# Performance work log

Measured on AMD Instinct MI355X. Metric: run time of the kernel, lower is better.

## Reference

```python
import jax, jax.numpy as jnp
import numpy as np

N, E, H, HEADS, NC, BLK = 100000, 1600000, 128, 4, 8192, 128

def _layernorm(x, g, b, eps=1e-5):
    m = jnp.mean(x, axis=-1, keepdims=True)
    v = jnp.var(x, axis=-1, keepdims=True)
    return (x - m) * jax.lax.rsqrt(v + eps) * g + b

def setup_inputs() -> dict:
    key = jax.random.key(0)
    ks = jax.random.split(key, 24)
    s = 0.05
    p = lambda k, shp: jax.random.normal(k, shp, jnp.float32) * s
    return {
        'x': jax.random.normal(ks[0], (N, H), jnp.float32),
        'ea': jax.random.normal(ks[1], (E, H), jnp.float32),
        # GINEConv edge linear (edge_dim -> hidden)
        'We': p(ks[2], (H, H)), 'be_': p(ks[3], (H,)),
        # GINEConv mlp: Linear(H,H) -> ReLU -> Linear(H,H)
        'W1': p(ks[4], (H, H)), 'b1': p(ks[5], (H,)),
        'W2': p(ks[6], (H, H)), 'b2': p(ks[7], (H,)),
        'ln1_g': jnp.ones((H,), jnp.float32), 'ln1_b': jnp.zeros((H,), jnp.float32),
        # MultiheadAttention packed qkv + out proj
        'in_w': p(ks[8], (3 * H, H)), 'in_b': p(ks[9], (3 * H,)),
        'out_w': p(ks[10], (H, H)), 'out_b': p(ks[11], (H,)),
        'ln2_g': jnp.ones((H,), jnp.float32), 'ln2_b': jnp.zeros((H,), jnp.float32),
        # FFN: Linear(H,2H) -> ReLU -> Linear(2H,H)
        'f1_w': p(ks[12], (2 * H, H)), 'f1_b': p(ks[13], (2 * H,)),
        'f2_w': p(ks[14], (H, 2 * H)), 'f2_b': p(ks[15], (H,)),
        'ei': jax.random.randint(ks[16], (2, E), 0, N, jnp.int64),
        'chem_idx': jnp.arange(NC, dtype=jnp.int64),
        'B': BLK,
    }

def reference(x, ea, We, be_, W1, b1, W2, b2, ln1_g, ln1_b, in_w, in_b,
              out_w, out_b, ln2_g, ln2_b, f1_w, f1_b, f2_w, f2_b,
              ei, chem_idx, B):
    n = x.shape[0]
    # ---- GINEConv: out_i = mlp((1+eps)*x_i + sum_j relu(x_j + lin(e_ji))), eps=0 ----
    src, dst = ei[0], ei[1]
    msg = jax.nn.relu(x[src] + ea @ We.T + be_)          # [E, H]
    agg = jax.ops.segment_sum(msg, dst, num_segments=n)  # [N, H]
    h = agg + x
    h = jax.nn.relu(h @ W1.T + b1) @ W2.T + b2
    x = _layernorm(x + h, ln1_g, ln1_b)
    # ---- chunked self-attention over chem nodes (chunks of size B) ----
    xc = x[chem_idx].reshape(-1, B, x.shape[-1])         # [nc, B, H]
    nc, _, hid = xc.shape
    dh = hid // HEADS
    qkv = xc @ in_w.T + in_b                             # [nc, B, 3H]
    q, k, v = jnp.split(qkv, 3, axis=-1)
    sp = lambda t: t.reshape(nc, B, HEADS, dh)
    att = jax.nn.softmax(jnp.einsum('bqhd,bkhd->bhqk', sp(q), sp(k)) * (1.0 / np.sqrt(dh)).astype(np.float32), axis=-1)
    o = jnp.einsum('bhqk,bkhd->bqhd', att, sp(v)).reshape(nc, B, hid)
    xc = xc + (o @ out_w.T + out_b)                      # residual inside BlockMHA
    xc = xc.reshape(-1, hid)
    # ---- FFN on chem subset ----
    h2 = _layernorm(xc, ln2_g, ln2_b)
    xc = xc + (jax.nn.relu(h2 @ f1_w.T + f1_b) @ f2_w.T + f2_b)
    return x.at[chem_idx].set(xc)
```

## Files before the change

kernel.cpp:

```cpp
#include <hip/hip_runtime.h>
#include <hip/hip_bf16.h>
#include <math.h>

typedef __attribute__((ext_vector_type(8))) __bf16 bf16x8;
typedef __attribute__((ext_vector_type(4))) float f32x4;
typedef __attribute__((ext_vector_type(4))) unsigned short u16x4;

#define HD  128
#define LDP 136

__device__ __forceinline__ unsigned short f2bf(float f) {
  __bf16 h = (__bf16)f;
  union { __bf16 h; unsigned short u; } v; v.h = h; return v.u;
}
__device__ __forceinline__ float bf2f(unsigned short h) {
  union { unsigned u; float f; } v; v.u = ((unsigned)h) << 16; return v.f;
}

__device__ __forceinline__ int idx_at(const void* p, long long i, int is64) {
  if (is64) return (int)((const long long*)p)[i];
  return ((const int*)p)[i];
}

__device__ __forceinline__ void mfma_tile_128(const unsigned short* a_s,
                                              const unsigned short* w_s,
                                              int w, int l15, int lg,
                                              f32x4 acc[2][8]) {
#pragma unroll
  for (int kk = 0; kk < 4; ++kk) {
    bf16x8 a[2], b[8];
#pragma unroll
    for (int mt = 0; mt < 2; ++mt)
      a[mt] = *(const bf16x8*)&a_s[(w * 32 + mt * 16 + l15) * LDP + kk * 32 + lg * 8];
#pragma unroll
    for (int nt = 0; nt < 8; ++nt)
      b[nt] = *(const bf16x8*)&w_s[(nt * 16 + l15) * LDP + kk * 32 + lg * 8];
#pragma unroll
    for (int mt = 0; mt < 2; ++mt)
#pragma unroll
      for (int nt = 0; nt < 8; ++nt)
        acc[mt][nt] = __builtin_amdgcn_mfma_f32_16x16x32_bf16(a[mt], b[nt], acc[mt][nt], 0, 0, 0);
  }
}

__device__ __forceinline__ void mfma_tile_gb(const unsigned short* a_s,
                                             const unsigned short* Wb,
                                             int w, int l15, int lg,
                                             f32x4 acc[2][8]) {
#pragma unroll
  for (int kk = 0; kk < 4; ++kk) {
    bf16x8 a[2], b[8];
#pragma unroll
    for (int mt = 0; mt < 2; ++mt)
      a[mt] = *(const bf16x8*)&a_s[(w * 32 + mt * 16 + l15) * LDP + kk * 32 + lg * 8];
#pragma unroll
    for (int nt = 0; nt < 8; ++nt)
      b[nt] = *(const bf16x8*)&Wb[(nt * 16 + l15) * 128 + kk * 32 + lg * 8];
#pragma unroll
    for (int mt = 0; mt < 2; ++mt)
#pragma unroll
      for (int nt = 0; nt < 8; ++nt)
        acc[mt][nt] = __builtin_amdgcn_mfma_f32_16x16x32_bf16(a[mt], b[nt], acc[mt][nt], 0, 0, 0);
  }
}

__device__ __forceinline__ void stage_f32s(unsigned short* dst, const float* src,
                                           long long src_ld, int tid, int T) {
  for (int i = tid; i < 128 * 32; i += T) {
    int r = i >> 5, c = (i & 31) << 2;
    float4 f = *(const float4*)&src[(long long)r * src_ld + c];
    u16x4 h = { f2bf(f.x), f2bf(f.y), f2bf(f.z), f2bf(f.w) };
    *(u16x4*)&dst[r * LDP + c] = h;
  }
}

__global__ void detect_idx_kernel(const void* __restrict__ ei, int E, int N,
                                  int* __restrict__ flag) {
  if (threadIdx.x == 0 && blockIdx.x == 0) {
    const long long* p = (const long long*)ei;
    int is64 = 1;
    long long step = E / 64; if (step < 1) step = 1;
    for (int i = 0; i < 64; ++i) {
      long long v = p[i * step];
      if (v < 0 || v >= N) { is64 = 0; break; }
    }
    *flag = is64;
  }
}

__global__ __launch_bounds__(256) void conv_we_kernel(const float* __restrict__ We,
                                                      unsigned short* __restrict__ we_bf) {
  int i = blockIdx.x * 256 + threadIdx.x;
  if (i < 128 * 128) {
    int r = i >> 7, c = i & 127;
    we_bf[r * 136 + c] = f2bf(We[i]);
  }
}
__global__ __launch_bounds__(256) void conv_w_kernel(const float* __restrict__ W,
                                                     unsigned short* __restrict__ out,
                                                     int n) {
  int i = blockIdx.x * 256 + threadIdx.x;
  if (i < n) out[i] = f2bf(W[i]);
}

__global__ __launch_bounds__(256) void hist_kernel(const void* __restrict__ ei,
                                                   const int* __restrict__ flag,
                                                   int* __restrict__ deg, int E) {
  const int is64 = *flag;
  for (long long e = blockIdx.x * 256LL + threadIdx.x; e < E;
       e += (long long)gridDim.x * 256)
    atomicAdd(&deg[idx_at(ei, (long long)E + e, is64)], 1);
}

#define SCH 1024
__global__ __launch_bounds__(256) void scan_a(const int* __restrict__ deg,
                                              int* __restrict__ bsum, int N) {
  const int b = blockIdx.x, t = threadIdx.x;
  int p = 0;
#pragma unroll
  for (int k = 0; k < 4; ++k) {
    int idx = b * SCH + t * 4 + k;
    if (idx < N) p += deg[idx];
  }
  __shared__ int warr[4];
  for (int o = 32; o > 0; o >>= 1) p += __shfl_xor(p, o);
  if ((t & 63) == 0) warr[t >> 6] = p;
  __syncthreads();
  if (t == 0) bsum[b] = warr[0] + warr[1] + warr[2] + warr[3];
}
__global__ void scan_b(int* __restrict__ bsum, int* __restrict__ off, int NB, int N) {
  if (threadIdx.x == 0 && blockIdx.x == 0) {
    int run = 0;
    for (int b = 0; b < NB; ++b) { int t = bsum[b]; bsum[b] = run; run += t; }
    off[N] = run;
  }
}
__global__ __launch_bounds__(256) void scan_c(const int* __restrict__ deg,
                                              const int* __restrict__ bsum,
                                              int* __restrict__ off,
                                              int* __restrict__ cursor, int N) {
  const int b = blockIdx.x, t = threadIdx.x;
  int d[4], s = 0;
#pragma unroll
  for (int k = 0; k < 4; ++k) {
    int idx = b * SCH + t * 4 + k;
    d[k] = (idx < N) ? deg[idx] : 0;
    s += d[k];
  }
  __shared__ int arr[256];
  arr[t] = s;
  __syncthreads();
  for (int stp = 1; stp < 256; stp <<= 1) {
    int v = (t >= stp) ? arr[t - stp] : 0;
    __syncthreads();
    arr[t] += v;
    __syncthreads();
  }
  int base = bsum[b] + arr[t] - s;
  int acc = 0;
#pragma unroll
  for (int k = 0; k < 4; ++k) {
    int idx = b * SCH + t * 4 + k;
    if (idx < N) { off[idx] = base + acc; cursor[idx] = base + acc; }
    acc += d[k];
  }
}

__global__ __launch_bounds__(256, 4) void edge_kernel8(
    const float* __restrict__ x, const float* __restrict__ ea,
    const unsigned short* __restrict__ we_bf, const float* __restrict__ be,
    const void* __restrict__ ei, const int* __restrict__ flag,
    int* __restrict__ cursor, unsigned short* __restrict__ msg, int E) {
  __shared__ unsigned short we_s[128 * LDP];
  __shared__ int s_src[128];
  __shared__ int s_pos[128];
  const int tid = threadIdx.x;
  const long long e0 = (long long)blockIdx.x * 128;
  const int is64 = *flag;

  if (tid < 128) {
    long long e = e0 + tid;
    int s = 0, p = 0;
    if (e < E) {
      s = idx_at(ei, e, is64);
      int d = idx_at(ei, (long long)E + e, is64);
      p = atomicAdd(&cursor[d], 1);
    }
    s_src[tid] = s; s_pos[tid] = p;
  }

  const int lane = tid & 63, w = tid >> 6;
  const int l15 = lane & 15, lg = lane >> 4;

  float4 af[2][4][2];
#pragma unroll
  for (int mt = 0; mt < 2; ++mt) {
    long long row = e0 + w * 32 + mt * 16 + l15;
    const float* src = &ea[(row < E ? row : e0) * HD + lg * 8];
#pragma unroll
    for (int kk = 0; kk < 4; ++kk) {
      af[mt][kk][0] = *(const float4*)&src[kk * 32];
      af[mt][kk][1] = *(const float4*)&src[kk * 32 + 4];
    }
  }

  for (int i = tid; i < 2048; i += 256) {
    int r = i >> 4, c = (i & 15) << 3;
    *(float4*)&we_s[r * LDP + c] = *(const float4*)&we_bf[r * 136 + c];
  }

  bf16x8 a[2][4];
#pragma unroll
  for (int mt = 0; mt < 2; ++mt)
#pragma unroll
    for (int kk = 0; kk < 4; ++kk) {
      float4 f0 = af[mt][kk][0], f1 = af[mt][kk][1];
      bf16x8 t;
      t[0] = (__bf16)f0.x; t[1] = (__bf16)f0.y; t[2] = (__bf16)f0.z; t[3] = (__bf16)f0.w;
      t[4] = (__bf16)f1.x; t[5] = (__bf16)f1.y; t[6] = (__bf16)f1.z; t[7] = (__bf16)f1.w;
      a[mt][kk] = t;
    }
  __syncthreads();

  f32x4 acc[2][8];
#pragma unroll
  for (int mt = 0; mt < 2; ++mt)
#pragma unroll
    for (int nt = 0; nt < 8; ++nt) acc[mt][nt] = (f32x4){0.f, 0.f, 0.f, 0.f};

#pragma unroll
  for (int kk = 0; kk < 4; ++kk) {
    bf16x8 b[8];
#pragma unroll
    for (int nt = 0; nt < 8; ++nt)
      b[nt] = *(const bf16x8*)&we_s[(nt * 16 + l15) * LDP + kk * 32 + lg * 8];
#pragma unroll
    for (int mt = 0; mt < 2; ++mt)
#pragma unroll
      for (int nt = 0; nt < 8; ++nt)
        acc[mt][nt] = __builtin_amdgcn_mfma_f32_16x16x32_bf16(a[mt][kk], b[nt], acc[mt][nt], 0, 0, 0);
  }

  float bev[8];
#pragma unroll
  for (int nt = 0; nt < 8; ++nt) bev[nt] = be[nt * 16 + l15];
  __syncthreads();

#pragma unroll
  for (int mt = 0; mt < 2; ++mt)
#pragma unroll
    for (int r = 0; r < 4; ++r) {
      int m = w * 32 + mt * 16 + lg * 4 + r;
#pragma unroll
      for (int nt = 0; nt < 8; ++nt)
        we_s[m * LDP + nt * 16 + l15] = f2bf(acc[mt][nt][r] + bev[nt]);
    }
  __syncthreads();

  for (int i = tid; i < 128 * 16; i += 256) {
    int r = i >> 4, sg = i & 15;
    if (e0 + r >= E) continue;
    const float* xrow = x + (size_t)s_src[r] * HD + sg * 8;
    float4 x0 = *(const float4*)&xrow[0];
    float4 x1 = *(const float4*)&xrow[4];
    bf16x8 g = *(const bf16x8*)&we_s[r * LDP + sg * 8];
    float v0 = (float)g[0] + x0.x, v1 = (float)g[1] + x0.y;
    float v2 = (float)g[2] + x0.z, v3 = (float)g[3] + x0.w;
    float v4 = (float)g[4] + x1.x, v5 = (float)g[5] + x1.y;
    float v6 = (float)g[6] + x1.z, v7 = (float)g[7] + x1.w;
    u16x4 h0 = { f2bf(v0 > 0.f ? v0 : 0.f), f2bf(v1 > 0.f ? v1 : 0.f),
                 f2bf(v2 > 0.f ? v2 : 0.f), f2bf(v3 > 0.f ? v3 : 0.f) };
    u16x4 h1 = { f2bf(v4 > 0.f ? v4 : 0.f), f2bf(v5 > 0.f ? v5 : 0.f),
                 f2bf(v6 > 0.f ? v6 : 0.f), f2bf(v7 > 0.f ? v7 : 0.f) };
    unsigned short* mp = &msg[(size_t)s_pos[r] * 128 + sg * 8];
    *(u16x4*)&mp[0] = h0;
    *(u16x4*)&mp[4] = h1;
  }
}

__global__ __launch_bounds__(256, 3) void node_kernel7(
    const float* __restrict__ x, float* __restrict__ xo,
    const int* __restrict__ off, const unsigned short* __restrict__ msg,
    const unsigned short* __restrict__ W1b, const float* __restrict__ b1,
    const unsigned short* __restrict__ W2b, const float* __restrict__ b2,
    const float* __restrict__ g1, const float* __restrict__ bt1, int N) {
  __shared__ unsigned short a_s[128 * LDP];
  const int tid = threadIdx.x;
  const long long r0 = (long long)blockIdx.x * 128;

  const int grp = tid >> 4, li = tid & 15;
  for (int r = grp; r < 128; r += 16) {
    long long gr = r0 + r;
    float a8[8] = {0.f, 0.f, 0.f, 0.f, 0.f, 0.f, 0.f, 0.f};
    if (gr < N) {
      float4 x0 = *(const float4*)&x[(size_t)gr * HD + li * 8];
      float4 x1 = *(const float4*)&x[(size_t)gr * HD + li * 8 + 4];
      a8[0] = x0.x; a8[1] = x0.y; a8[2] = x0.z; a8[3] = x0.w;
      a8[4] = x1.x; a8[5] = x1.y; a8[6] = x1.z; a8[7] = x1.w;
      const int j0 = off[gr], j1 = off[gr + 1];
      int j = j0;
      for (; j + 3 < j1; j += 4) {
        const u16x4* p0 = (const u16x4*)&msg[(size_t)j * 128 + li * 8];
        const u16x4* p1 = (const u16x4*)&msg[(size_t)(j + 1) * 128 + li * 8];
        const u16x4* p2 = (const u16x4*)&msg[(size_t)(j + 2) * 128 + li * 8];
        const u16x4* p3 = (const u16x4*)&msg[(size_t)(j + 3) * 128 + li * 8];
        u16x4 v0 = p0[0], v1 = p0[1], v2 = p1[0], v3 = p1[1];
        u16x4 v4 = p2[0], v5 = p2[1], v6 = p3[0], v7 = p3[1];
#pragma unroll
        for (int k = 0; k < 4; ++k) {
          a8[k]     += (bf2f(v0[k]) + bf2f(v2[k])) + (bf2f(v4[k]) + bf2f(v6[k]));
          a8[4 + k] += (bf2f(v1[k]) + bf2f(v3[k])) + (bf2f(v5[k]) + bf2f(v7[k]));
        }
      }
      for (; j < j1; ++j) {
        const u16x4* p0 = (const u16x4*)&msg[(size_t)j * 128 + li * 8];
        u16x4 v0 = p0[0], v1 = p0[1];
#pragma unroll
        for (int k = 0; k < 4; ++k) { a8[k] += bf2f(v0[k]); a8[4 + k] += bf2f(v1[k]); }
      }
    }
    u16x4 h0 = { f2bf(a8[0]), f2bf(a8[1]), f2bf(a8[2]), f2bf(a8[3]) };
    u16x4 h1 = { f2bf(a8[4]), f2bf(a8[5]), f2bf(a8[6]), f2bf(a8[7]) };
    *(u16x4*)&a_s[r * LDP + li * 8] = h0;
    *(u16x4*)&a_s[r * LDP + li * 8 + 4] = h1;
  }
  __syncthreads();

  const int lane = tid & 63, w = tid >> 6;
  const int l15 = lane & 15, lg = lane >> 4;
  f32x4 acc[2][8];
#pragma unroll
  for (int mt = 0; mt < 2; ++mt)
#pragma unroll
    for (int nt = 0; nt < 8; ++nt) acc[mt][nt] = (f32x4){0.f, 0.f, 0.f, 0.f};
  mfma_tile_gb(a_s, W1b, w, l15, lg, acc);
  __syncthreads();

#pragma unroll
  for (int mt = 0; mt < 2; ++mt)
#pragma unroll
    for (int r = 0; r < 4; ++r) {
      int m = w * 32 + mt * 16 + lg * 4 + r;
#pragma unroll
      for (int nt = 0; nt < 8; ++nt) {
        int n = nt * 16 + l15;
        float t = acc[mt][nt][r] + b1[n];
        a_s[m * LDP + n] = f2bf(t > 0.f ? t : 0.f);
      }
    }
  __syncthreads();

  f32x4 acc2[2][8];
#pragma unroll
  for (int mt = 0; mt < 2; ++mt)
#pragma unroll
    for (int nt = 0; nt < 8; ++nt) acc2[mt][nt] = (f32x4){0.f, 0.f, 0.f, 0.f};
  mfma_tile_gb(a_s, W2b, w, l15, lg, acc2);
  __syncthreads();

#pragma unroll
  for (int mt = 0; mt < 2; ++mt)
#pragma unroll
    for (int r = 0; r < 4; ++r) {
      int m = w * 32 + mt * 16 + lg * 4 + r;
      if (r0 + m < N) {
#pragma unroll
        for (int nt = 0; nt < 8; ++nt) {
          int n = nt * 16 + l15;
          a_s[m * LDP + n] = f2bf(x[(r0 + m) * HD + n] + acc2[mt][nt][r] + b2[n]);
        }
      }
    }
  __syncthreads();

  for (int row = w; row < 128; row += 4) {
    if (r0 + row >= N) continue;
    float v1 = bf2f(a_s[row * LDP + lane]), v2 = bf2f(a_s[row * LDP + 64 + lane]);
    float s = v1 + v2, sq = v1 * v1 + v2 * v2;
    for (int o = 32; o > 0; o >>= 1) { s += __shfl_xor(s, o); sq += __shfl_xor(sq, o); }
    float mean = s * (1.f / 128.f);
    float var = sq * (1.f / 128.f) - mean * mean;
    float rs = rsqrtf(var + 1e-5f);
    xo[(r0 + row) * HD + lane]      = (v1 - mean) * rs * g1[lane] + bt1[lane];
    xo[(r0 + row) * HD + 64 + lane] = (v2 - mean) * rs * g1[lane + 64] + bt1[lane + 64];
  }
}

__global__ __launch_bounds__(256) void edge_kernel(
    const float* __restrict__ x, const float* __restrict__ ea,
    const float* __restrict__ We, const float* __restrict__ be,
    const void* __restrict__ ei, const int* __restrict__ flag,
    float* __restrict__ agg, int E, int N) {
  __shared__ unsigned short ea_s[128 * LDP];
  __shared__ unsigned short we_s[128 * LDP];
  __shared__ int s_src[128];
  __shared__ int s_dst[128];
  const int tid = threadIdx.x;
  const long long e0 = (long long)blockIdx.x * 128;
  const int is64 = *flag;
  if (tid < 128) {
    long long e = e0 + tid;
    int s = 0, d = 0;
    if (e < E) { s = idx_at(ei, e, is64); d = idx_at(ei, (long long)E + e, is64); }
    s_src[tid] = s; s_dst[tid] = d;
  }
  for (int i = tid; i < 128 * 32; i += 256) {
    int r = i >> 5, c = (i & 31) << 2;
    float4 f = {0.f, 0.f, 0.f, 0.f};
    if (e0 + r < E) f = *(const float4*)&ea[(e0 + r) * HD + c];
    u16x4 h = { f2bf(f.x), f2bf(f.y), f2bf(f.z), f2bf(f.w) };
    *(u16x4*)&ea_s[r * LDP + c] = h;
    float4 g = *(const float4*)&We[r * HD + c];
    u16x4 hw = { f2bf(g.x), f2bf(g.y), f2bf(g.z), f2bf(g.w) };
    *(u16x4*)&we_s[r * LDP + c] = hw;
  }
  __syncthreads();
  const int lane = tid & 63, w = tid >> 6;
  const int l15 = lane & 15, lg = lane >> 4;
  f32x4 acc[2][8];
#pragma unroll
  for (int mt = 0; mt < 2; ++mt)
#pragma unroll
    for (int nt = 0; nt < 8; ++nt) acc[mt][nt] = (f32x4){0.f, 0.f, 0.f, 0.f};
  mfma_tile_128(ea_s, we_s, w, l15, lg, acc);
  float bev[8];
#pragma unroll
  for (int nt = 0; nt < 8; ++nt) bev[nt] = be[nt * 16 + l15];
#pragma unroll
  for (int mt = 0; mt < 2; ++mt) {
#pragma unroll
    for (int r = 0; r < 4; ++r) {
      int m = w * 32 + mt * 16 + lg * 4 + r;
      if (e0 + m >= E) continue;
      const float* xrow = x + (size_t)s_src[m] * HD;
      float* arow = agg + (size_t)s_dst[m] * HD;
#pragma unroll
      for (int nt = 0; nt < 8; ++nt) {
        int n = nt * 16 + l15;
        float val = acc[mt][nt][r] + bev[nt] + xrow[n];
        if (val > 0.f) unsafeAtomicAdd(&arow[n], val);
      }
    }
  }
}

__global__ __launch_bounds__(256) void node_kernel(
    const float* __restrict__ x, float* xo,
    const float* __restrict__ W1, const float* __restrict__ b1,
    const float* __restrict__ W2, const float* __restrict__ b2,
    const float* __restrict__ g1, const float* __restrict__ bt1, int N) {
  __shared__ char smem[2 * 128 * LDP * 2];
  unsigned short* a_s = (unsigned short*)smem;
  unsigned short* w_s = (unsigned short*)smem + 128 * LDP;
  float* y_s = (float*)smem;
  const int tid = threadIdx.x;
  const long long r0 = (long long)blockIdx.x * 128;
  for (int i = tid; i < 128 * 32; i += 256) {
    int r = i >> 5, c = (i & 31) << 2;
    float4 f = {0.f, 0.f, 0.f, 0.f};
    if (r0 + r < N) {
      float4 xa = *(const float4*)&x[(r0 + r) * HD + c];
      float4 ag = *(const float4*)&xo[(r0 + r) * HD + c];
      f.x = xa.x + ag.x; f.y = xa.y + ag.y; f.z = xa.z + ag.z; f.w = xa.w + ag.w;
    }
    u16x4 h = { f2bf(f.x), f2bf(f.y), f2bf(f.z), f2bf(f.w) };
    *(u16x4*)&a_s[r * LDP + c] = h;
    float4 g = *(const float4*)&W1[r * HD + c];
    u16x4 hw = { f2bf(g.x), f2bf(g.y), f2bf(g.z), f2bf(g.w) };
    *(u16x4*)&w_s[r * LDP + c] = hw;
  }
  __syncthreads();
  const int lane = tid & 63, w = tid >> 6;
  const int l15 = lane & 15, lg = lane >> 4;
  f32x4 acc[2][8];
#pragma unroll
  for (int mt = 0; mt < 2; ++mt)
#pragma unroll
    for (int nt = 0; nt < 8; ++nt) acc[mt][nt] = (f32x4){0.f, 0.f, 0.f, 0.f};
  mfma_tile_128(a_s, w_s, w, l15, lg, acc);
  __syncthreads();
#pragma unroll
  for (int mt = 0; mt < 2; ++mt)
#pragma unroll
    for (int r = 0; r < 4; ++r) {
      int m = w * 32 + mt * 16 + lg * 4 + r;
#pragma unroll
      for (int nt = 0; nt < 8; ++nt) {
        int n = nt * 16 + l15;
        float t = acc[mt][nt][r] + b1[n];
        a_s[m * LDP + n] = f2bf(t > 0.f ? t : 0.f);
      }
    }
  stage_f32s(w_s, W2, HD, tid, 256);
  __syncthreads();
  f32x4 acc2[2][8];
#pragma unroll
  for (int mt = 0; mt < 2; ++mt)
#pragma unroll
    for (int nt = 0; nt < 8; ++nt) acc2[mt][nt] = (f32x4){0.f, 0.f, 0.f, 0.f};
  mfma_tile_128(a_s, w_s, w, l15, lg, acc2);
  __syncthreads();
#pragma unroll
  for (int mt = 0; mt < 2; ++mt)
#pragma unroll
    for (int r = 0; r < 4; ++r) {
      int m = w * 32 + mt * 16 + lg * 4 + r;
      if (r0 + m < N) {
#pragma unroll
        for (int nt = 0; nt < 8; ++nt) {
          int n = nt * 16 + l15;
          y_s[m * 132 + n] = x[(r0 + m) * HD + n] + acc2[mt][nt][r] + b2[n];
        }
      }
    }
  __syncthreads();
  for (int row = w; row < 128; row += 4) {
    if (r0 + row >= N) continue;
    float v1 = y_s[row * 132 + lane], v2 = y_s[row * 132 + 64 + lane];
    float s = v1 + v2, sq = v1 * v1 + v2 * v2;
    for (int o = 32; o > 0; o >>= 1) { s += __shfl_xor(s, o); sq += __shfl_xor(sq, o); }
    float mean = s * (1.f / 128.f);
    float var = sq * (1.f / 128.f) - mean * mean;
    float rs = rsqrtf(var + 1e-5f);
    xo[(r0 + row) * HD + lane]      = (v1 - mean) * rs * g1[lane] + bt1[lane];
    xo[(r0 + row) * HD + 64 + lane] = (v2 - mean) * rs * g1[lane + 64] + bt1[lane + 64];
  }
}

__global__ __launch_bounds__(256) void qkv_kernel(
    const float* __restrict__ xo, const float* __restrict__ in_w,
    const float* __restrict__ in_b, const void* __restrict__ chem,
    const int* __restrict__ flag, float* __restrict__ qkv) {
  __shared__ unsigned short a_s[128 * LDP];
  __shared__ unsigned short w_s[128 * LDP];
  __shared__ int s_row[128];
  const int tid = threadIdx.x;
  const int chunk = blockIdx.x, sec = blockIdx.y;
  const int is64 = *flag;
  if (tid < 128) s_row[tid] = idx_at(chem, (long long)chunk * 128 + tid, is64);
  __syncthreads();
  for (int i = tid; i < 128 * 32; i += 256) {
    int r = i >> 5, c = (i & 31) << 2;
    float4 f = *(const float4*)&xo[(size_t)s_row[r] * HD + c];
    u16x4 h = { f2bf(f.x), f2bf(f.y), f2bf(f.z), f2bf(f.w) };
    *(u16x4*)&a_s[r * LDP + c] = h;
    float4 g = *(const float4*)&in_w[(size_t)(sec * 128 + r) * HD + c];
    u16x4 hw = { f2bf(g.x), f2bf(g.y), f2bf(g.z), f2bf(g.w) };
    *(u16x4*)&w_s[r * LDP + c] = hw;
  }
  __syncthreads();
  const int lane = tid & 63, w = tid >> 6;
  const int l15 = lane & 15, lg = lane >> 4;
  f32x4 acc[2][8];
#pragma unroll
  for (int mt = 0; mt < 2; ++mt)
#pragma unroll
    for (int nt = 0; nt < 8; ++nt) acc[mt][nt] = (f32x4){0.f, 0.f, 0.f, 0.f};
  mfma_tile_128(a_s, w_s, w, l15, lg, acc);
#pragma unroll
  for (int mt = 0; mt < 2; ++mt)
#pragma unroll
    for (int r = 0; r < 4; ++r) {
      int m = w * 32 + mt * 16 + lg * 4 + r;
#pragma unroll
      for (int nt = 0; nt < 8; ++nt) {
        int n = nt * 16 + l15;
        qkv[(size_t)(chunk * 128 + m) * 384 + sec * 128 + n] = acc[mt][nt][r] + in_b[sec * 128 + n];
      }
    }
}

__global__ __launch_bounds__(128) void attn_kernel(const float* __restrict__ qkv,
                                                   float* __restrict__ o) {
  __shared__ float k_s[128 * 32];
  __shared__ float v_s[128 * 32];
  const int tid = threadIdx.x;
  const int chunk = blockIdx.x, h = blockIdx.y;
  const float scale = 0.1767766952966369f;
  for (int i = tid; i < 128 * 32; i += 128) {
    int r = i >> 5, d = i & 31;
    k_s[i] = qkv[(size_t)(chunk * 128 + r) * 384 + 128 + h * 32 + d];
    v_s[i] = qkv[(size_t)(chunk * 128 + r) * 384 + 256 + h * 32 + d];
  }
  float qr[32];
  const int m = tid;
#pragma unroll
  for (int d = 0; d < 32; ++d)
    qr[d] = qkv[(size_t)(chunk * 128 + m) * 384 + h * 32 + d] * scale;
  __syncthreads();
  float mx = -1e30f, sm = 0.f;
  for (int j = 0; j < 128; ++j) {
    float s = 0.f;
#pragma unroll
    for (int d = 0; d < 32; ++d) s += qr[d] * k_s[j * 32 + d];
    if (s > mx) { sm = sm * __expf(mx - s); mx = s; }
    sm += __expf(s - mx);
  }
  const float inv = 1.f / sm;
  float ov[32];
#pragma unroll
  for (int d = 0; d < 32; ++d) ov[d] = 0.f;
  for (int j = 0; j < 128; ++j) {
    float s = 0.f;
#pragma unroll
    for (int d = 0; d < 32; ++d) s += qr[d] * k_s[j * 32 + d];
    float p = __expf(s - mx) * inv;
#pragma unroll
    for (int d = 0; d < 32; ++d) ov[d] += p * v_s[j * 32 + d];
  }
#pragma unroll
  for (int d = 0; d < 32; ++d)
    o[(size_t)(chunk * 128 + m) * HD + h * 32 + d] = ov[d];
}

__global__ __launch_bounds__(256) void oproj_kernel(
    const float* __restrict__ xo, const float* __restrict__ o,
    const float* __restrict__ Wo, const float* __restrict__ bo,
    const float* __restrict__ g2, const float* __restrict__ bt2,
    const void* __restrict__ chem, const int* __restrict__ flag,
    float* __restrict__ xc2, unsigned short* __restrict__ h2b) {
  __shared__ char smem[2 * 128 * LDP * 2];
  unsigned short* a_s = (unsigned short*)smem;
  unsigned short* w_s = (unsigned short*)smem + 128 * LDP;
  float* y_s = (float*)smem;
  __shared__ int s_row[128];
  const int tid = threadIdx.x;
  const int chunk = blockIdx.x;
  const int is64 = *flag;
  if (tid < 128) s_row[tid] = idx_at(chem, (long long)chunk * 128 + tid, is64);
  stage_f32s(a_s, o + (size_t)chunk * 128 * HD, HD, tid, 256);
  stage_f32s(w_s, Wo, HD, tid, 256);
  __syncthreads();
  const int lane = tid & 63, w = tid >> 6;
  const int l15 = lane & 15, lg = lane >> 4;
  f32x4 acc[2][8];
#pragma unroll
  for (int mt = 0; mt < 2; ++mt)
#pragma unroll
    for (int nt = 0; nt < 8; ++nt) acc[mt][nt] = (f32x4){0.f, 0.f, 0.f, 0.f};
  mfma_tile_128(a_s, w_s, w, l15, lg, acc);
  __syncthreads();
#pragma unroll
  for (int mt = 0; mt < 2; ++mt)
#pragma unroll
    for (int r = 0; r < 4; ++r) {
      int m = w * 32 + mt * 16 + lg * 4 + r;
#pragma unroll
      for (int nt = 0; nt < 8; ++nt) {
        int n = nt * 16 + l15;
        y_s[m * 132 + n] = xo[(size_t)s_row[m] * HD + n] + acc[mt][nt][r] + bo[n];
      }
    }
  __syncthreads();
  for (int row = w; row < 128; row += 4) {
    float v1 = y_s[row * 132 + lane], v2 = y_s[row * 132 + 64 + lane];
    float s = v1 + v2, sq = v1 * v1 + v2 * v2;
    for (int o2 = 32; o2 > 0; o2 >>= 1) { s += __shfl_xor(s, o2); sq += __shfl_xor(sq, o2); }
    float mean = s * (1.f / 128.f);
    float var = sq * (1.f / 128.f) - mean * mean;
    float rs = rsqrtf(var + 1e-5f);
    size_t gi = (size_t)(chunk * 128 + row) * HD;
    xc2[gi + lane] = v1; xc2[gi + 64 + lane] = v2;
    h2b[gi + lane]      = f2bf((v1 - mean) * rs * g2[lane] + bt2[lane]);
    h2b[gi + 64 + lane] = f2bf((v2 - mean) * rs * g2[lane + 64] + bt2[lane + 64]);
  }
}

__global__ __launch_bounds__(256) void ffn1_kernel(
    const unsigned short* __restrict__ h2b, const float* __restrict__ f1w,
    const float* __restrict__ f1b, unsigned short* __restrict__ u) {
  __shared__ unsigned short a_s[128 * LDP];
  __shared__ unsigned short w_s[128 * LDP];
  const int tid = threadIdx.x;
  const int chunk = blockIdx.x, sec = blockIdx.y;
  for (int i = tid; i < 128 * 32; i += 256) {
    int r = i >> 5, c = (i & 31) << 2;
    *(u16x4*)&a_s[r * LDP + c] = *(const u16x4*)&h2b[(size_t)(chunk * 128 + r) * HD + c];
  }
  stage_f32s(w_s, f1w + (size_t)sec * 128 * HD, HD, tid, 256);
  __syncthreads();
  const int lane = tid & 63, w = tid >> 6;
  const int l15 = lane & 15, lg = lane >> 4;
  f32x4 acc[2][8];
#pragma unroll
  for (int mt = 0; mt < 2; ++mt)
#pragma unroll
    for (int nt = 0; nt < 8; ++nt) acc[mt][nt] = (f32x4){0.f, 0.f, 0.f, 0.f};
  mfma_tile_128(a_s, w_s, w, l15, lg, acc);
#pragma unroll
  for (int mt = 0; mt < 2; ++mt)
#pragma unroll
    for (int r = 0; r < 4; ++r) {
      int m = w * 32 + mt * 16 + lg * 4 + r;
#pragma unroll
      for (int nt = 0; nt < 8; ++nt) {
        int n = nt * 16 + l15;
        float t = acc[mt][nt][r] + f1b[sec * 128 + n];
        u[(size_t)(chunk * 128 + m) * 256 + sec * 128 + n] = f2bf(t > 0.f ? t : 0.f);
      }
    }
}

__global__ __launch_bounds__(256) void ffn2_kernel(
    const unsigned short* __restrict__ u, const float* __restrict__ f2w,
    const float* __restrict__ f2b, const float* __restrict__ xc2,
    const void* __restrict__ chem, const int* __restrict__ flag,
    float* __restrict__ out) {
  __shared__ unsigned short a_s[128 * LDP];
  __shared__ unsigned short w_s[128 * LDP];
  __shared__ int s_row[128];
  const int tid = threadIdx.x;
  const int chunk = blockIdx.x;
  const int is64 = *flag;
  if (tid < 128) s_row[tid] = idx_at(chem, (long long)chunk * 128 + tid, is64);
  const int lane = tid & 63, w = tid >> 6;
  const int l15 = lane & 15, lg = lane >> 4;
  f32x4 acc[2][8];
#pragma unroll
  for (int mt = 0; mt < 2; ++mt)
#pragma unroll
    for (int nt = 0; nt < 8; ++nt) acc[mt][nt] = (f32x4){0.f, 0.f, 0.f, 0.f};
  for (int half = 0; half < 2; ++half) {
    __syncthreads();
    for (int i = tid; i < 128 * 32; i += 256) {
      int r = i >> 5, c = (i & 31) << 2;
      *(u16x4*)&a_s[r * LDP + c] =
          *(const u16x4*)&u[(size_t)(chunk * 128 + r) * 256 + half * 128 + c];
      float4 g = *(const float4*)&f2w[(size_t)r * 256 + half * 128 + c];
      u16x4 hw = { f2bf(g.x), f2bf(g.y), f2bf(g.z), f2bf(g.w) };
      *(u16x4*)&w_s[r * LDP + c] = hw;
    }
    __syncthreads();
    mfma_tile_128(a_s, w_s, w, l15, lg, acc);
  }
#pragma unroll
  for (int mt = 0; mt < 2; ++mt)
#pragma unroll
    for (int r = 0; r < 4; ++r) {
      int m = w * 32 + mt * 16 + lg * 4 + r;
#pragma unroll
      for (int nt = 0; nt < 8; ++nt) {
        int n = nt * 16 + l15;
        float val = xc2[(size_t)(chunk * 128 + m) * HD + n] + acc[mt][nt][r] + f2b[n];
        out[(size_t)s_row[m] * HD + n] = val;
      }
    }
}

extern "C" void kernel_launch(void* const* d_in, const int* in_sizes, int n_in,
                              void* d_out, int out_size, void* d_ws, size_t ws_size,
                              hipStream_t stream) {
  const float* x    = (const float*)d_in[0];
  const float* ea   = (const float*)d_in[1];
  const float* We   = (const float*)d_in[2];
  const float* be   = (const float*)d_in[3];
  const float* W1   = (const float*)d_in[4];
  const float* b1   = (const float*)d_in[5];
  const float* W2   = (const float*)d_in[6];
  const float* b2   = (const float*)d_in[7];
  const float* g1   = (const float*)d_in[8];
  const float* bt1  = (const float*)d_in[9];
  const float* in_w = (const float*)d_in[10];
  const float* in_b = (const float*)d_in[11];
  const float* outw = (const float*)d_in[12];
  const float* outb = (const float*)d_in[13];
  const float* g2   = (const float*)d_in[14];
  const float* bt2  = (const float*)d_in[15];
  const float* f1w  = (const float*)d_in[16];
  const float* f1b  = (const float*)d_in[17];
  const float* f2w  = (const float*)d_in[18];
  const float* f2b  = (const float*)d_in[19];
  const void*  ei   = d_in[20];
  const void*  chem = d_in[21];
  const int N  = in_sizes[0] / HD;
  const int E  = in_sizes[1] / HD;
  const int NC = in_sizes[21];
  const int NB = (N + SCH - 1) / SCH;
  float* xo = (float*)d_out;

  char* ws = (char*)d_ws;
  size_t o = 0;
  auto alloc = [&](size_t bytes) { size_t p = o; o = (o + bytes + 255) & ~255ULL; return p; };
  size_t o_qkv  = alloc((size_t)NC * 384 * 4);
  size_t o_obuf = alloc((size_t)NC * 128 * 4);
  size_t o_xc2  = alloc((size_t)NC * 128 * 4);
  size_t o_h2b  = alloc((size_t)NC * 128 * 2);
  size_t o_ubuf = alloc((size_t)NC * 256 * 2);
  size_t o_flag = alloc(4);
  size_t o_webf = alloc(128 * 136 * 2);
  size_t o_w1b  = alloc(128 * 128 * 2);
  size_t o_w2b  = alloc(128 * 128 * 2);
  size_t o_deg  = alloc((size_t)N * 4);
  size_t o_off  = alloc((size_t)(N + 1) * 4);
  size_t o_cur  = alloc((size_t)N * 4);
  size_t o_bsum = alloc((size_t)NB * 4);
  size_t o_msg  = alloc((size_t)E * 128 * 2);
  size_t need = o;

  float*          qkv  = (float*)(ws + o_qkv);
  float*          obuf = (float*)(ws + o_obuf);
  float*          xc2  = (float*)(ws + o_xc2);
  unsigned short* h2b  = (unsigned short*)(ws + o_h2b);
  unsigned short* ubuf = (unsigned short*)(ws + o_ubuf);
  int*            flag = (int*)(ws + o_flag);
  unsigned short* webf = (unsigned short*)(ws + o_webf);
  unsigned short* w1b  = (unsigned short*)(ws + o_w1b);
  unsigned short* w2b  = (unsigned short*)(ws + o_w2b);
  int*            deg  = (int*)(ws + o_deg);
  int*            off  = (int*)(ws + o_off);
  int*            cur  = (int*)(ws + o_cur);
  int*            bsum = (int*)(ws + o_bsum);
  unsigned short* msg  = (unsigned short*)(ws + o_msg);

  detect_idx_kernel<<<1, 64, 0, stream>>>(ei, E, N, flag);

  if (ws_size >= need) {
    hipMemsetAsync(deg, 0, (size_t)N * 4, stream);
    hist_kernel<<<dim3(1024), 256, 0, stream>>>(ei, flag, deg, E);
    scan_a<<<dim3(NB), 256, 0, stream>>>(deg, bsum, N);
    scan_b<<<1, 64, 0, stream>>>(bsum, off, NB, N);
    scan_c<<<dim3(NB), 256, 0, stream>>>(deg, bsum, off, cur, N);
    conv_we_kernel<<<dim3(64), 256, 0, stream>>>(We, webf);
    conv_w_kernel<<<dim3(64), 256, 0, stream>>>(W1, w1b, 128 * 128);
    conv_w_kernel<<<dim3(64), 256, 0, stream>>>(W2, w2b, 128 * 128);
    edge_kernel8<<<dim3((E + 127) / 128), 256, 0, stream>>>(x, ea, webf, be, ei, flag,
                                                            cur, msg, E);
    node_kernel7<<<dim3((N + 127) / 128), 256, 0, stream>>>(x, xo, off, msg, w1b, b1,
                                                            w2b, b2, g1, bt1, N);
  } else {
    hipMemsetAsync(xo, 0, (size_t)N * HD * sizeof(float), stream);
    edge_kernel<<<dim3((E + 127) / 128), 256, 0, stream>>>(x, ea, We, be, ei, flag, xo, E, N);
    node_kernel<<<dim3((N + 127) / 128), 256, 0, stream>>>(x, xo, W1, b1, W2, b2, g1, bt1, N);
  }

  const int ncs = NC / 128;
  qkv_kernel<<<dim3(ncs, 3), 256, 0, stream>>>(xo, in_w, in_b, chem, flag, qkv);
  attn_kernel<<<dim3(ncs, 4), 128, 0, stream>>>(qkv, obuf);
  oproj_kernel<<<dim3(ncs), 256, 0, stream>>>(xo, obuf, outw, outb, g2, bt2, chem, flag, xc2, h2b);
  ffn1_kernel<<<dim3(ncs, 2), 256, 0, stream>>>(h2b, f1w, f1b, ubuf);
  ffn2_kernel<<<dim3(ncs), 256, 0, stream>>>(ubuf, f2w, f2b, xc2, chem, flag, xo);
}
```

Before: 781.7 us.

## Use bf16 copy of x for edge gather and split node aggregation from MLP

Converts x to bf16 once so the per-edge random gather of source rows reads half as many bytes. The segment-sum aggregation moves out of the MLP node kernel into a separate gather kernel with many small blocks, which writes a bf16 h buffer that the MLP kernel then loads at higher occupancy. The serial block-sum scan is replaced with a parallel single-block scan. The cost is extra kernels and an extra round trip of an N×128 bf16 buffer, and the self term x is now added in bf16 rather than fp32.

New measurement: 732.7 us. 6.3% less time.

```diff
diff --git a/kernel.cpp b/kernel.cpp
--- a/kernel.cpp
+++ b/kernel.cpp
@@ -102,6 +102,19 @@
   int i = blockIdx.x * 256 + threadIdx.x;
   if (i < n) out[i] = f2bf(W[i]);
 }
+__global__ __launch_bounds__(256) void conv_x_kernel(const float* __restrict__ x,
+                                                     unsigned short* __restrict__ xb,
+                                                     long long n8) {
+  long long i = blockIdx.x * 256LL + threadIdx.x;
+  if (i < n8) {
+    float4 f0 = *(const float4*)&x[i * 8];
+    float4 f1 = *(const float4*)&x[i * 8 + 4];
+    u16x4 h0 = { f2bf(f0.x), f2bf(f0.y), f2bf(f0.z), f2bf(f0.w) };
+    u16x4 h1 = { f2bf(f1.x), f2bf(f1.y), f2bf(f1.z), f2bf(f1.w) };
+    *(u16x4*)&xb[i * 8] = h0;
+    *(u16x4*)&xb[i * 8 + 4] = h1;
+  }
+}
 
 __global__ __launch_bounds__(256) void hist_kernel(const void* __restrict__ ei,
                                                    const int* __restrict__ flag,
@@ -135,6 +148,22 @@
     off[N] = run;
   }
 }
+__global__ __launch_bounds__(128) void scan_b2(int* __restrict__ bsum,
+                                               int* __restrict__ off, int NB, int N) {
+  __shared__ int arr[128];
+  const int t = threadIdx.x;
+  int v = (t < NB) ? bsum[t] : 0;
+  arr[t] = v;
+  __syncthreads();
+  for (int s = 1; s < 128; s <<= 1) {
+    int u = (t >= s) ? arr[t - s] : 0;
+    __syncthreads();
+    arr[t] += u;
+    __syncthreads();
+  }
+  if (t < NB) bsum[t] = arr[t] - v;
+  if (t == 0) off[N] = arr[127];
+}
 __global__ __launch_bounds__(256) void scan_c(const int* __restrict__ deg,
                                               const int* __restrict__ bsum,
                                               int* __restrict__ off,
@@ -166,8 +195,8 @@
   }
 }
 
-__global__ __launch_bounds__(256, 4) void edge_kernel8(
-    const float* __restrict__ x, const float* __restrict__ ea,
+__global__ __launch_bounds__(256, 4) void edge_kernel9(
+    const unsigned short* __restrict__ x_bf, const float* __restrict__ ea,
     const unsigned short* __restrict__ we_bf, const float* __restrict__ be,
     const void* __restrict__ ei, const int* __restrict__ flag,
     int* __restrict__ cursor, unsigned short* __restrict__ msg, int E) {
@@ -260,27 +289,63 @@
   for (int i = tid; i < 128 * 16; i += 256) {
     int r = i >> 4, sg = i & 15;
     if (e0 + r >= E) continue;
-    const float* xrow = x + (size_t)s_src[r] * HD + sg * 8;
-    float4 x0 = *(const float4*)&xrow[0];
-    float4 x1 = *(const float4*)&xrow[4];
+    bf16x8 xv = *(const bf16x8*)&x_bf[(size_t)s_src[r] * HD + sg * 8];
     bf16x8 g = *(const bf16x8*)&we_s[r * LDP + sg * 8];
-    float v0 = (float)g[0] + x0.x, v1 = (float)g[1] + x0.y;
-    float v2 = (float)g[2] + x0.z, v3 = (float)g[3] + x0.w;
-    float v4 = (float)g[4] + x1.x, v5 = (float)g[5] + x1.y;
-    float v6 = (float)g[6] + x1.z, v7 = (float)g[7] + x1.w;
-    u16x4 h0 = { f2bf(v0 > 0.f ? v0 : 0.f), f2bf(v1 > 0.f ? v1 : 0.f),
-                 f2bf(v2 > 0.f ? v2 : 0.f), f2bf(v3 > 0.f ? v3 : 0.f) };
-    u16x4 h1 = { f2bf(v4 > 0.f ? v4 : 0.f), f2bf(v5 > 0.f ? v5 : 0.f),
-                 f2bf(v6 > 0.f ? v6 : 0.f), f2bf(v7 > 0.f ? v7 : 0.f) };
+    u16x4 h0, h1;
+#pragma unroll
+    for (int k = 0; k < 4; ++k) {
+      float v = (float)g[k] + (float)xv[k];
+      h0[k] = f2bf(v > 0.f ? v : 0.f);
+    }
+#pragma unroll
+    for (int k = 0; k < 4; ++k) {
+      float v = (float)g[4 + k] + (float)xv[4 + k];
+      h1[k] = f2bf(v > 0.f ? v : 0.f);
+    }
     unsigned short* mp = &msg[(size_t)s_pos[r] * 128 + sg * 8];
     *(u16x4*)&mp[0] = h0;
     *(u16x4*)&mp[4] = h1;
   }
 }
 
-__global__ __launch_bounds__(256, 3) void node_kernel7(
+__global__ __launch_bounds__(256) void gather_kernel(
+    const unsigned short* __restrict__ x_bf, const int* __restrict__ off,
+    const unsigned short* __restrict__ msg, unsigned short* __restrict__ h_bf,
+    int N) {
+  const int tid = threadIdx.x;
+  const int grp = tid >> 4, li = tid & 15;
+  const long long row = (long long)blockIdx.x * 16 + grp;
+  if (row >= N) return;
+  const int co = li * 8;
+  float a8[8];
+  bf16x8 xv = *(const bf16x8*)&x_bf[row * HD + co];
+#pragma unroll
+  for (int k = 0; k < 8; ++k) a8[k] = (float)xv[k];
+  const int j0 = off[row], j1 = off[row + 1];
+  int j = j0;
+  for (; j + 3 < j1; j += 4) {
+    bf16x8 v0 = *(const bf16x8*)&msg[(size_t)j * 128 + co];
+    bf16x8 v1 = *(const bf16x8*)&msg[(size_t)(j + 1) * 128 + co];
+    bf16x8 v2 = *(const bf16x8*)&msg[(size_t)(j + 2) * 128 + co];
+    bf16x8 v3 = *(const bf16x8*)&msg[(size_t)(j + 3) * 128 + co];
+#pragma unroll
+    for (int k = 0; k < 8; ++k)
+      a8[k] += ((float)v0[k] + (float)v1[k]) + ((float)v2[k] + (float)v3[k]);
+  }
+  for (; j < j1; ++j) {
+    bf16x8 v0 = *(const bf16x8*)&msg[(size_t)j * 128 + co];
+#pragma unroll
+    for (int k = 0; k < 8; ++k) a8[k] += (float)v0[k];
+  }
+  bf16x8 hv;
+#pragma unroll
+  for (int k = 0; k < 8; ++k) hv[k] = (__bf16)a8[k];
+  *(bf16x8*)&h_bf[row * HD + co] = hv;
+}
+
+__global__ __launch_bounds__(256, 4) void mlp_kernel(
     const float* __restrict__ x, float* __restrict__ xo,
-    const int* __restrict__ off, const unsigned short* __restrict__ msg,
+    const unsigned short* __restrict__ h_bf,
     const unsigned short* __restrict__ W1b, const float* __restrict__ b1,
     const unsigned short* __restrict__ W2b, const float* __restrict__ b2,
     const float* __restrict__ g1, const float* __restrict__ bt1, int N) {
@@ -288,41 +353,16 @@
   const int tid = threadIdx.x;
   const long long r0 = (long long)blockIdx.x * 128;
 
-  const int grp = tid >> 4, li = tid & 15;
-  for (int r = grp; r < 128; r += 16) {
+  for (int i = tid; i < 2048; i += 256) {
+    int r = i >> 4, c = (i & 15) << 3;
     long long gr = r0 + r;
-    float a8[8] = {0.f, 0.f, 0.f, 0.f, 0.f, 0.f, 0.f, 0.f};
-    if (gr < N) {
-      float4 x0 = *(const float4*)&x[(size_t)gr * HD + li * 8];
-      float4 x1 = *(const float4*)&x[(size_t)gr * HD + li * 8 + 4];
-      a8[0] = x0.x; a8[1] = x0.y; a8[2] = x0.z; a8[3] = x0.w;
-      a8[4] = x1.x; a8[5] = x1.y; a8[6] = x1.z; a8[7] = x1.w;
-      const int j0 = off[gr], j1 = off[gr + 1];
-      int j = j0;
-      for (; j + 3 < j1; j += 4) {
-        const u16x4* p0 = (const u16x4*)&msg[(size_t)j * 128 + li * 8];
-        const u16x4* p1 = (const u16x4*)&msg[(size_t)(j + 1) * 128 + li * 8];
-        const u16x4* p2 = (const u16x4*)&msg[(size_t)(j + 2) * 128 + li * 8];
-        const u16x4* p3 = (const u16x4*)&msg[(size_t)(j + 3) * 128 + li * 8];
-        u16x4 v0 = p0[0], v1 = p0[1], v2 = p1[0], v3 = p1[1];
-        u16x4 v4 = p2[0], v5 = p2[1], v6 = p3[0], v7 = p3[1];
-#pragma unroll
-        for (int k = 0; k < 4; ++k) {
-          a8[k]     += (bf2f(v0[k]) + bf2f(v2[k])) + (bf2f(v4[k]) + bf2f(v6[k]));
-          a8[4 + k] += (bf2f(v1[k]) + bf2f(v3[k])) + (bf2f(v5[k]) + bf2f(v7[k]));
-        }
-      }
-      for (; j < j1; ++j) {
-        const u16x4* p0 = (const u16x4*)&msg[(size_t)j * 128 + li * 8];
-        u16x4 v0 = p0[0], v1 = p0[1];
-#pragma unroll
-        for (int k = 0; k < 4; ++k) { a8[k] += bf2f(v0[k]); a8[4 + k] += bf2f(v1[k]); }
-      }
-    }
-    u16x4 h0 = { f2bf(a8[0]), f2bf(a8[1]), f2bf(a8[2]), f2bf(a8[3]) };
-    u16x4 h1 = { f2bf(a8[4]), f2bf(a8[5]), f2bf(a8[6]), f2bf(a8[7]) };
-    *(u16x4*)&a_s[r * LDP + li * 8] = h0;
-    *(u16x4*)&a_s[r * LDP + li * 8 + 4] = h1;
+    bf16x8 v;
+    if (gr < N) v = *(const bf16x8*)&h_bf[gr * HD + c];
+    else {
+#pragma unroll
+      for (int k = 0; k < 8; ++k) v[k] = (__bf16)0.f;
+    }
+    *(bf16x8*)&a_s[r * LDP + c] = v;
   }
   __syncthreads();
 
@@ -790,6 +830,8 @@
   size_t o_webf = alloc(128 * 136 * 2);
   size_t o_w1b  = alloc(128 * 128 * 2);
   size_t o_w2b  = alloc(128 * 128 * 2);
+  size_t o_xbf  = alloc((size_t)N * 128 * 2);
+  size_t o_hbf  = alloc((size_t)N * 128 * 2);
   size_t o_deg  = alloc((size_t)N * 4);
   size_t o_off  = alloc((size_t)(N + 1) * 4);
   size_t o_cur  = alloc((size_t)N * 4);
@@ -806,6 +848,8 @@
   unsigned short* webf = (unsigned short*)(ws + o_webf);
   unsigned short* w1b  = (unsigned short*)(ws + o_w1b);
   unsigned short* w2b  = (unsigned short*)(ws + o_w2b);
+  unsigned short* xbf  = (unsigned short*)(ws + o_xbf);
+  unsigned short* hbf  = (unsigned short*)(ws + o_hbf);
   int*            deg  = (int*)(ws + o_deg);
   int*            off  = (int*)(ws + o_off);
   int*            cur  = (int*)(ws + o_cur);
@@ -816,17 +860,20 @@
 
   if (ws_size >= need) {
     hipMemsetAsync(deg, 0, (size_t)N * 4, stream);
+    conv_x_kernel<<<dim3((N * 16 + 255) / 256), 256, 0, stream>>>(x, xbf, (long long)N * 16);
     hist_kernel<<<dim3(1024), 256, 0, stream>>>(ei, flag, deg, E);
     scan_a<<<dim3(NB), 256, 0, stream>>>(deg, bsum, N);
-    scan_b<<<1, 64, 0, stream>>>(bsum, off, NB, N);
+    if (NB <= 128) scan_b2<<<1, 128, 0, stream>>>(bsum, off, NB, N);
+    else           scan_b<<<1, 64, 0, stream>>>(bsum, off, NB, N);
     scan_c<<<dim3(NB), 256, 0, stream>>>(deg, bsum, off, cur, N);
     conv_we_kernel<<<dim3(64), 256, 0, stream>>>(We, webf);
     conv_w_kernel<<<dim3(64), 256, 0, stream>>>(W1, w1b, 128 * 128);
     conv_w_kernel<<<dim3(64), 256, 0, stream>>>(W2, w2b, 128 * 128);
-    edge_kernel8<<<dim3((E + 127) / 128), 256, 0, stream>>>(x, ea, webf, be, ei, flag,
-                                                            cur, msg, E);
-    node_kernel7<<<dim3((N + 127) / 128), 256, 0, stream>>>(x, xo, off, msg, w1b, b1,
-                                                            w2b, b2, g1, bt1, N);
+    edge_kernel9<<<dim3((E + 127) / 128), 256, 0, stream>>>(xbf, ea, webf, be, ei,
+                                                            flag, cur, msg, E);
+    gather_kernel<<<dim3((N + 15) / 16), 256, 0, stream>>>(xbf, off, msg, hbf, N);
+    mlp_kernel<<<dim3((N + 127) / 128), 256, 0, stream>>>(x, xo, hbf, w1b, b1, w2b,
+                                                          b2, g1, bt1, N);
   } else {
     hipMemsetAsync(xo, 0, (size_t)N * HD * sizeof(float), stream);
     edge_kernel<<<dim3((E + 127) / 128), 256, 0, stream>>>(x, ea, We, be, ei, flag, xo, E, N);
```
